# Optimization experiments

Hardware: AMD Instinct MI355X
Metric: run time of the kernel (lower is better)

Reference implementation:

```python
import jax, jax.numpy as jnp
import numpy as np

F, C, H, W_DIM, B = 64, 1024, 32, 32, 64

def setup_inputs() -> dict:
    key = jax.random.key(0)
    k1, k2, k3 = jax.random.split(key, 3)
    x = jax.random.normal(k1, (B, F, H, W_DIM), dtype=jnp.float32)
    # nn.Linear default init: U(-1/sqrt(in), 1/sqrt(in)) for weight [out,in] and bias
    bound = 1.0 / np.sqrt(C)
    weight = jax.random.uniform(k2, (F, C, C), minval=-bound, maxval=bound, dtype=jnp.float32)
    bias = jax.random.uniform(k3, (F, C), minval=-bound, maxval=bound, dtype=jnp.float32)
    return {"x": x, "weight": weight, "bias": bias}

def reference(x, weight, bias):
    # x: [B, F, H, W]; per-feature Linear over flattened HxW (C = H*W)
    b, f, h, w = x.shape
    xf = x.reshape(b, f, h * w)                      # [B, F, C]
    # torch Linear: y = x @ W.T + b, W is [out, in] -> contract over 'in' axis
    y = jnp.einsum('bfc,foc->bfo', xf, weight) + bias  # [B, F, C]
    return y.reshape(b, f, h, w)
```

## Files before the change

### kernel.cpp

```cpp
#include <hip/hip_runtime.h>
#include <hip/hip_bf16.h>

#define F_DIM 64
#define B_DIM 64
#define C_DIM 1024
#define BM 64
#define BN 128
#define BK 64
#define NT (C_DIM / BK)
#define NTILES (C_DIM / BN)
#define THREADS 512

using f32x4  = __attribute__((ext_vector_type(4))) float;
using bf16x8 = __attribute__((ext_vector_type(8))) short;
using s16x4  = __attribute__((ext_vector_type(4))) short;

static __device__ __forceinline__ short f2bf(float f) {
    unsigned u = __float_as_uint(f);
    unsigned r = (u + 0x7fffu + ((u >> 16) & 1u)) >> 16;
    return (short)r;
}

__global__ __launch_bounds__(THREADS, 4)
void channelfc_kernel(const float* __restrict__ x,
                      const float* __restrict__ w,
                      const float* __restrict__ bias,
                      float* __restrict__ out)
{
    const int n    = blockIdx.x;
    const int xcd  = n & 7;
    const int j    = n >> 3;
    const int f    = xcd + 8 * (j >> 3);
    const int bx   = j & 7;
    const int ocol0 = bx * BN;

    const int tid   = threadIdx.x;
    const int lane  = tid & 63;
    const int wid   = tid >> 6;
    const int wr    = wid >> 2;
    const int wc    = wid & 3;

    __shared__ short sA[2][BM * BK];
    __shared__ short sB[2][BN * BK];

    const float* xA = x + (size_t)f * C_DIM;
    const float* wB = w + ((size_t)f * C_DIM + ocol0) * C_DIM;

    f32x4 ra[2];
    f32x4 rb[4];

    auto load_tile = [&](int t) {
        const int k0 = t * BK;
        #pragma unroll
        for (int i = 0; i < 2; ++i) {
            int id = i * THREADS + tid, row = id >> 4, k4 = id & 15;
            ra[i] = *(const f32x4*)(xA + (size_t)row * (F_DIM * C_DIM) + k0 + k4 * 4);
        }
        #pragma unroll
        for (int i = 0; i < 4; ++i) {
            int id = i * THREADS + tid, row = id >> 4, k4 = id & 15;
            rb[i] = *(const f32x4*)(wB + (size_t)row * C_DIM + k0 + k4 * 4);
        }
    };

    auto store_tile = [&](int buf) {
        #pragma unroll
        for (int i = 0; i < 2; ++i) {
            int id = i * THREADS + tid, row = id >> 4, k4 = id & 15;
            int byte = (k4 * 8) ^ ((row & 7) << 4);
            s16x4 v; v[0]=f2bf(ra[i][0]); v[1]=f2bf(ra[i][1]); v[2]=f2bf(ra[i][2]); v[3]=f2bf(ra[i][3]);
            *(s16x4*)((char*)&sA[buf][0] + row * 128 + byte) = v;
        }
        #pragma unroll
        for (int i = 0; i < 4; ++i) {
            int id = i * THREADS + tid, row = id >> 4, k4 = id & 15;
            int byte = (k4 * 8) ^ ((row & 7) << 4);
            s16x4 v; v[0]=f2bf(rb[i][0]); v[1]=f2bf(rb[i][1]); v[2]=f2bf(rb[i][2]); v[3]=f2bf(rb[i][3]);
            *(s16x4*)((char*)&sB[buf][0] + row * 128 + byte) = v;
        }
    };

    f32x4 acc[2][2] = {};

    auto compute = [&](int buf) {
        #pragma unroll
        for (int ks = 0; ks < 2; ++ks) {
            const int kbyte = ks * 64 + (lane >> 4) * 16;
            bf16x8 af[2], bfr[2];
            #pragma unroll
            for (int mt = 0; mt < 2; ++mt) {
                int row = wr * 32 + mt * 16 + (lane & 15);
                af[mt] = *(const bf16x8*)((const char*)&sA[buf][0] + row * 128 + (kbyte ^ ((row & 7) << 4)));
            }
            #pragma unroll
            for (int nt = 0; nt < 2; ++nt) {
                int row = wc * 32 + nt * 16 + (lane & 15);
                bfr[nt] = *(const bf16x8*)((const char*)&sB[buf][0] + row * 128 + (kbyte ^ ((row & 7) << 4)));
            }
            #pragma unroll
            for (int mt = 0; mt < 2; ++mt)
                #pragma unroll
                for (int nt = 0; nt < 2; ++nt)
                    acc[mt][nt] = __builtin_amdgcn_mfma_f32_16x16x32_bf16(af[mt], bfr[nt], acc[mt][nt], 0, 0, 0);
        }
    };

    load_tile(0);
    for (int t = 0; t < NT; ++t) {
        const int buf = t & 1;
        store_tile(buf);
        if (t + 1 < NT) load_tile(t + 1);
        __syncthreads();
        compute(buf);
    }

    const int ncol_base = ocol0 + wc * 32 + (lane & 15);
    const int mrow_base = wr * 32 + (lane >> 4) * 4;
    #pragma unroll
    for (int nt = 0; nt < 2; ++nt) {
        const int o  = ncol_base + nt * 16;
        const float bv = bias[f * C_DIM + o];
        #pragma unroll
        for (int mt = 0; mt < 2; ++mt) {
            #pragma unroll
            for (int r = 0; r < 4; ++r) {
                const int b = mrow_base + mt * 16 + r;
                out[((size_t)b * F_DIM + f) * C_DIM + o] = acc[mt][nt][r] + bv;
            }
        }
    }
}

extern "C" void kernel_launch(void* const* d_in, const int* in_sizes, int n_in,
                              void* d_out, int out_size, void* d_ws, size_t ws_size,
                              hipStream_t stream) {
    const float* x    = (const float*)d_in[0];
    const float* w    = (const float*)d_in[1];
    const float* bias = (const float*)d_in[2];
    float* out        = (float*)d_out;
    channelfc_kernel<<<dim3(NTILES * F_DIM), dim3(THREADS), 0, stream>>>(x, w, bias, out);
}
```

Baseline: 58.32 us.

## Stage full X slice in LDS once and process two output tiles per block

Each block now loads its feature's whole 64x1024 input slice into shared memory as bf16 once, then loops over two 128-column output tiles, streaming weight tiles through a register-prefetched double buffer. The grid drops from 512 to 256 blocks, and the per-tile reload and conversion of X is removed. The cost is a 128KB LDS footprint for X, which allows only one block per CU, plus half as many blocks and an up-front X-load phase that is not overlapped with compute. Latency hiding also relies on a single wave group per CU.

```diff
diff --git a/kernel.cpp b/kernel.cpp
--- a/kernel.cpp
+++ b/kernel.cpp
@@ -4,11 +4,9 @@
 #define F_DIM 64
 #define B_DIM 64
 #define C_DIM 1024
-#define BM 64
 #define BN 128
 #define BK 64
-#define NT (C_DIM / BK)
-#define NTILES (C_DIM / BN)
+#define NSTEP 32
 #define THREADS 512
 
 using f32x4  = __attribute__((ext_vector_type(4))) float;
@@ -21,7 +19,7 @@
     return (short)r;
 }
 
-__global__ __launch_bounds__(THREADS, 4)
+__global__ __launch_bounds__(THREADS, 2)
 void channelfc_kernel(const float* __restrict__ x,
                       const float* __restrict__ w,
                       const float* __restrict__ bias,
@@ -29,73 +27,83 @@
 {
     const int n    = blockIdx.x;
     const int xcd  = n & 7;
-    const int j    = n >> 3;
-    const int f    = xcd + 8 * (j >> 3);
-    const int bx   = j & 7;
-    const int ocol0 = bx * BN;
+    const int loc  = n >> 3;
+    const int f    = xcd + 8 * (loc >> 2);
+    const int bx   = loc & 3;
 
-    const int tid   = threadIdx.x;
-    const int lane  = tid & 63;
-    const int wid   = tid >> 6;
-    const int wr    = wid >> 2;
-    const int wc    = wid & 3;
+    const int tid  = threadIdx.x;
+    const int lane = tid & 63;
+    const int wid  = tid >> 6;
+    const int wr   = wid >> 2;
+    const int wc   = wid & 3;
 
-    __shared__ short sA[2][BM * BK];
-    __shared__ short sB[2][BN * BK];
+    __shared__ short sX[B_DIM * C_DIM];
+    __shared__ short sW[2][BN * BK];
 
     const float* xA = x + (size_t)f * C_DIM;
-    const float* wB = w + ((size_t)f * C_DIM + ocol0) * C_DIM;
+    const float* wB = w + (size_t)f * C_DIM * C_DIM;
 
-    f32x4 ra[2];
-    f32x4 rb[4];
+    f32x4 rwA[4], rwB[4];
 
-    auto load_tile = [&](int t) {
-        const int k0 = t * BK;
-        #pragma unroll
-        for (int i = 0; i < 2; ++i) {
-            int id = i * THREADS + tid, row = id >> 4, k4 = id & 15;
-            ra[i] = *(const f32x4*)(xA + (size_t)row * (F_DIM * C_DIM) + k0 + k4 * 4);
-        }
+    auto loadW = [&](int s, f32x4 (&r)[4]) {
+        const int o0 = (bx * 2 + (s >> 4)) * BN;
+        const int k0 = (s & 15) * BK;
         #pragma unroll
         for (int i = 0; i < 4; ++i) {
             int id = i * THREADS + tid, row = id >> 4, k4 = id & 15;
-            rb[i] = *(const f32x4*)(wB + (size_t)row * C_DIM + k0 + k4 * 4);
+            r[i] = *(const f32x4*)(wB + (size_t)(o0 + row) * C_DIM + k0 + k4 * 4);
         }
     };
-
-    auto store_tile = [&](int buf) {
-        #pragma unroll
-        for (int i = 0; i < 2; ++i) {
-            int id = i * THREADS + tid, row = id >> 4, k4 = id & 15;
-            int byte = (k4 * 8) ^ ((row & 7) << 4);
-            s16x4 v; v[0]=f2bf(ra[i][0]); v[1]=f2bf(ra[i][1]); v[2]=f2bf(ra[i][2]); v[3]=f2bf(ra[i][3]);
-            *(s16x4*)((char*)&sA[buf][0] + row * 128 + byte) = v;
-        }
+    auto storeW = [&](int buf, const f32x4 (&r)[4]) {
         #pragma unroll
         for (int i = 0; i < 4; ++i) {
             int id = i * THREADS + tid, row = id >> 4, k4 = id & 15;
             int byte = (k4 * 8) ^ ((row & 7) << 4);
-            s16x4 v; v[0]=f2bf(rb[i][0]); v[1]=f2bf(rb[i][1]); v[2]=f2bf(rb[i][2]); v[3]=f2bf(rb[i][3]);
-            *(s16x4*)((char*)&sB[buf][0] + row * 128 + byte) = v;
+            s16x4 v; v[0]=f2bf(r[i][0]); v[1]=f2bf(r[i][1]); v[2]=f2bf(r[i][2]); v[3]=f2bf(r[i][3]);
+            *(s16x4*)((char*)&sW[buf][0] + row * 128 + byte) = v;
         }
     };
 
+    loadW(0, rwA);
+    loadW(1, rwB);
+    #pragma unroll 1
+    for (int c8 = 0; c8 < 4; ++c8) {
+        f32x4 tx[8];
+        #pragma unroll
+        for (int i = 0; i < 8; ++i) {
+            int id = (c8 * 8 + i) * THREADS + tid;
+            int row = id >> 8, k4 = id & 255;
+            tx[i] = *(const f32x4*)(xA + (size_t)row * (F_DIM * C_DIM) + k4 * 4);
+        }
+        #pragma unroll
+        for (int i = 0; i < 8; ++i) {
+            int id = (c8 * 8 + i) * THREADS + tid;
+            int row = id >> 8, k4 = id & 255;
+            int byte = (k4 * 8) ^ ((row & 7) << 4);
+            s16x4 v; v[0]=f2bf(tx[i][0]); v[1]=f2bf(tx[i][1]); v[2]=f2bf(tx[i][2]); v[3]=f2bf(tx[i][3]);
+            *(s16x4*)((char*)&sX[0] + row * 2048 + byte) = v;
+        }
+    }
+    storeW(0, rwA);
+    __syncthreads();
+
     f32x4 acc[2][2] = {};
 
-    auto compute = [&](int buf) {
+    auto compute = [&](int buf, int s) {
         #pragma unroll
         for (int ks = 0; ks < 2; ++ks) {
-            const int kbyte = ks * 64 + (lane >> 4) * 16;
+            const int kx = (s & 15) * 128 + ks * 64 + (lane >> 4) * 16;
+            const int kw = ks * 64 + (lane >> 4) * 16;
             bf16x8 af[2], bfr[2];
             #pragma unroll
             for (int mt = 0; mt < 2; ++mt) {
                 int row = wr * 32 + mt * 16 + (lane & 15);
-                af[mt] = *(const bf16x8*)((const char*)&sA[buf][0] + row * 128 + (kbyte ^ ((row & 7) << 4)));
+                af[mt] = *(const bf16x8*)((const char*)&sX[0] + row * 2048 + (kx ^ ((row & 7) << 4)));
             }
             #pragma unroll
             for (int nt = 0; nt < 2; ++nt) {
                 int row = wc * 32 + nt * 16 + (lane & 15);
-                bfr[nt] = *(const bf16x8*)((const char*)&sB[buf][0] + row * 128 + (kbyte ^ ((row & 7) << 4)));
+                bfr[nt] = *(const bf16x8*)((const char*)&sW[buf][0] + row * 128 + (kw ^ ((row & 7) << 4)));
             }
             #pragma unroll
             for (int mt = 0; mt < 2; ++mt)
@@ -105,30 +113,45 @@
         }
     };
 
-    load_tile(0);
-    for (int t = 0; t < NT; ++t) {
-        const int buf = t & 1;
-        store_tile(buf);
-        if (t + 1 < NT) load_tile(t + 1);
+    auto epilogue = [&](int p) {
+        const int ocol0 = (bx * 2 + p) * BN;
+        const int ncol_base = ocol0 + wc * 32 + (lane & 15);
+        const int mrow_base = wr * 32 + (lane >> 4) * 4;
+        #pragma unroll
+        for (int nt = 0; nt < 2; ++nt) {
+            const int o  = ncol_base + nt * 16;
+            const float bv = bias[f * C_DIM + o];
+            #pragma unroll
+            for (int mt = 0; mt < 2; ++mt)
+                #pragma unroll
+                for (int r = 0; r < 4; ++r) {
+                    const int b = mrow_base + mt * 16 + r;
+                    out[((size_t)b * F_DIM + f) * C_DIM + o] = acc[mt][nt][r] + bv;
+                }
+        }
+    };
+
+    #pragma unroll 1
+    for (int it = 0; it < 16; ++it) {
+        const int s = 2 * it;
+        if (s + 2 < NSTEP) loadW(s + 2, rwA);
+        storeW(1, rwB);
+        compute(0, s);
         __syncthreads();
-        compute(buf);
+        if (s + 3 < NSTEP) loadW(s + 3, rwB);
+        if (s + 2 < NSTEP) storeW(0, rwA);
+        compute(1, s + 1);
+        if (s + 1 == 15) {
+            epilogue(0);
+            #pragma unroll
+            for (int mt = 0; mt < 2; ++mt)
+                #pragma unroll
+                for (int nt = 0; nt < 2; ++nt)
+                    acc[mt][nt] = f32x4{0.f, 0.f, 0.f, 0.f};
+        }
+        __syncthreads();
     }
-
-    const int ncol_base = ocol0 + wc * 32 + (lane & 15);
-    const int mrow_base = wr * 32 + (lane >> 4) * 4;
-    #pragma unroll
-    for (int nt = 0; nt < 2; ++nt) {
-        const int o  = ncol_base + nt * 16;
-        const float bv = bias[f * C_DIM + o];
-        #pragma unroll
-        for (int mt = 0; mt < 2; ++mt) {
-            #pragma unroll
-            for (int r = 0; r < 4; ++r) {
-                const int b = mrow_base + mt * 16 + r;
-                out[((size_t)b * F_DIM + f) * C_DIM + o] = acc[mt][nt][r] + bv;
-            }
-        }
-    }
+    epilogue(1);
 }
 
 extern "C" void kernel_launch(void* const* d_in, const int* in_sizes, int n_in,
@@ -138,5 +161,5 @@
     const float* w    = (const float*)d_in[1];
     const float* bias = (const float*)d_in[2];
     float* out        = (float*)d_out;
-    channelfc_kernel<<<dim3(NTILES * F_DIM), dim3(THREADS), 0, stream>>>(x, w, bias, out);
+    channelfc_kernel<<<dim3(256), dim3(THREADS), 0, stream>>>(x, w, bias, out);
 }
```

After: 62.71 us. +7.5%, slower.
